# Optimization experiments

Hardware: AMD Instinct MI355X
Metric: run time of the kernel (lower is better)

## Reference

```python
import jax, jax.numpy as jnp
import numpy as np
from jax import lax

B, F, N, C = 1024, 256, 65536, 1000
SOURCE_CLASSES = 751
TEMP = 0.05
MOMENTUM = 0.2


def setup_inputs() -> dict:
    key = jax.random.key(0)
    k1, k2, k3, k4 = jax.random.split(key, 4)
    inputs = jax.random.normal(k1, (B, F), dtype=jnp.float32)
    # indexes in [1, N] so that (indexes - 1) are all valid -> the boolean mask
    # `inds = indexes >= 0` keeps every row (static shapes under jit)
    indexes = jax.random.randint(k2, (B,), 1, N + 1, dtype=jnp.int32)
    features = jax.random.normal(k3, (N, F), dtype=jnp.float32)
    features = features / jnp.linalg.norm(features, axis=1, keepdims=True)  # bank stores unit rows
    labels = jax.random.randint(k4, (N,), 0, C, dtype=jnp.int32)
    return {"inputs": inputs, "indexes": indexes, "features": features, "labels": labels}


def _forward(inputs, idx, features, labels):
    # F.normalize(inputs, dim=1)
    x = inputs / jnp.linalg.norm(inputs, axis=1, keepdims=True)           # [B, F]
    logits = (x @ features.T) / TEMP                                      # [B, N]
    targets = labels[idx]                                                 # [B]
    # sim.index_add_(0, labels, inputs.t()) -> per-class column sums
    sim = jax.ops.segment_sum(logits.T, labels, num_segments=C)           # [C, B]
    nums = jax.ops.segment_sum(jnp.ones((N,), jnp.float32), labels, num_segments=C)  # [C]
    mask = nums > 0
    sim = sim / jnp.where(mask, nums, 1.0)[:, None]                       # per-class mean
    # masked softmax over classes (faithful to original: plain exp, +eps denominator)
    exps = jnp.exp(sim.T) * mask[None, :].astype(jnp.float32)            # [B, C]
    p = exps / (exps.sum(axis=1, keepdims=True) + 1e-6)
    logp = jnp.log(p + 1e-6)
    # F.nll_loss(..., ignore_index=source_classes-1)
    valid = (targets != SOURCE_CLASSES - 1).astype(jnp.float32)
    nll = -jnp.take_along_axis(logp, targets[:, None], axis=1)[:, 0]
    loss = jnp.sum(nll * valid) / jnp.maximum(valid.sum(), 1.0)
    return loss, x


def reference(inputs, indexes, features, labels):
    idx = indexes - 1
    idx = jnp.where(idx == 5554, SOURCE_CLASSES - 1, idx)  # is_source=True special case
    loss, x = _forward(inputs, idx, features, labels)
    # HM.backward's per-sample sequential momentum scatter update + renorm of the bank.
    # Order-dependent on duplicate indices -> inherently sequential -> lax.scan.
    def step(feats, xy):
        xi, yi = xy
        row = MOMENTUM * feats[yi] + (1.0 - MOMENTUM) * xi
        row = row / jnp.linalg.norm(row)
        return feats.at[yi].set(row), None

    new_features, _ = lax.scan(step, features, (x, idx))
    return loss, new_features
```

## Files before the change

kernel.cpp:

```cpp
#include <hip/hip_runtime.h>
#include <math.h>

#define Bn   1024
#define Fdim 256
#define Nn   65536
#define Cn   1000
#define INV_TEMP 20.0f
#define MOM  0.2f

struct WS {
  float x[Bn * Fdim];
  float meanP[Fdim * Cn];
  float mask[Cn];
  float tExp[Bn];
  int   idx[Bn];
  int   targets[Bn];
  int   offsets[Cn];
  int   cursor[Cn];
  int   list[Nn];
  float meanC[Cn * Fdim];
  int   counts[Cn];
  float sumExp[Bn];
};

__global__ __launch_bounds__(64) void k1_norm(const float* __restrict__ inputs,
                                              const int* __restrict__ indexes,
                                              const int* __restrict__ labels,
                                              float* __restrict__ x,
                                              int* __restrict__ idx, int* __restrict__ targets) {
  int b = blockIdx.x, t = threadIdx.x;
  float4 v = *(const float4*)&inputs[b * Fdim + t * 4];
  float s = v.x * v.x + v.y * v.y + v.z * v.z + v.w * v.w;
#pragma unroll
  for (int o = 32; o > 0; o >>= 1) s += __shfl_xor(s, o, 64);
  float inv = 1.0f / sqrtf(s);
  v.x *= inv; v.y *= inv; v.z *= inv; v.w *= inv;
  *(float4*)&x[b * Fdim + t * 4] = v;
  if (t == 0) {
    int i0 = indexes[b] - 1;
    if (i0 == 5554) i0 = 750;
    idx[b] = i0;
    targets[b] = labels[i0];
  }
}

__global__ __launch_bounds__(256) void k2_count(const int* __restrict__ labels,
                                                int* __restrict__ counts) {
  int t = blockIdx.x * blockDim.x + threadIdx.x;
  int4 l = *(const int4*)&labels[t * 4];
  atomicAdd(&counts[l.x], 1);
  atomicAdd(&counts[l.y], 1);
  atomicAdd(&counts[l.z], 1);
  atomicAdd(&counts[l.w], 1);
}

__global__ void k3_scan(const int* __restrict__ counts, int* __restrict__ offsets,
                        int* __restrict__ cursor) {
  __shared__ int s[1024];
  int t = threadIdx.x;
  int v = (t < Cn) ? counts[t] : 0;
  s[t] = v;
  __syncthreads();
  for (int o = 1; o < 1024; o <<= 1) {
    int a = (t >= o) ? s[t - o] : 0;
    __syncthreads();
    s[t] += a;
    __syncthreads();
  }
  if (t < Cn) {
    int off = s[t] - v;
    offsets[t] = off;
    cursor[t] = off;
  }
}

__global__ __launch_bounds__(256) void k4_fill(const int* __restrict__ labels,
                                               int* __restrict__ cursor,
                                               int* __restrict__ list) {
  int t = blockIdx.x * blockDim.x + threadIdx.x;
  int4 l = *(const int4*)&labels[t * 4];
  int n = t * 4;
  list[atomicAdd(&cursor[l.x], 1)] = n;
  list[atomicAdd(&cursor[l.y], 1)] = n + 1;
  list[atomicAdd(&cursor[l.z], 1)] = n + 2;
  list[atomicAdd(&cursor[l.w], 1)] = n + 3;
}

__global__ __launch_bounds__(256) void k5_fused(const float* __restrict__ features,
                                                const int* __restrict__ list,
                                                const int* __restrict__ labels,
                                                float* __restrict__ meanC,
                                                float* __restrict__ out1) {
  int w = blockIdx.x * 4 + (threadIdx.x >> 6);
  int lane = threadIdx.x & 63;
  int e0 = w * 16;
  float4 acc = {0.f, 0.f, 0.f, 0.f};
  int cur = -1;
#pragma unroll
  for (int bh = 0; bh < 2; bh++) {
    int r[8], cc[8];
#pragma unroll
    for (int j = 0; j < 8; j++) r[j] = list[e0 + bh * 8 + j];
#pragma unroll
    for (int j = 0; j < 8; j++) cc[j] = labels[r[j]];
    float4 v[8];
#pragma unroll
    for (int j = 0; j < 8; j++)
      v[j] = *(const float4*)&features[r[j] * Fdim + lane * 4];
#pragma unroll
    for (int j = 0; j < 8; j++) {
      float* o = &out1[r[j] * Fdim + lane * 4];
      o[0] = v[j].x; o[1] = v[j].y; o[2] = v[j].z; o[3] = v[j].w;
      if (cc[j] != cur) {
        if (cur >= 0) {
          float* p = &meanC[cur * Fdim + lane * 4];
          atomicAdd(p + 0, acc.x); atomicAdd(p + 1, acc.y);
          atomicAdd(p + 2, acc.z); atomicAdd(p + 3, acc.w);
        }
        acc.x = 0.f; acc.y = 0.f; acc.z = 0.f; acc.w = 0.f;
        cur = cc[j];
      }
      acc.x += v[j].x; acc.y += v[j].y; acc.z += v[j].z; acc.w += v[j].w;
    }
  }
  float* p = &meanC[cur * Fdim + lane * 4];
  atomicAdd(p + 0, acc.x); atomicAdd(p + 1, acc.y);
  atomicAdd(p + 2, acc.z); atomicAdd(p + 3, acc.w);
}

__global__ __launch_bounds__(256) void k5t_pack(const float* __restrict__ meanC,
                                                const int* __restrict__ counts,
                                                float* __restrict__ meanP,
                                                float* __restrict__ mask) {
  int c = blockIdx.x, t = threadIdx.x;
  int cnt = counts[c];
  float rc = (cnt > 0) ? 1.0f / (float)cnt : 0.f;
  float s = meanC[c * Fdim + t];
  meanP[((t >> 2) * Cn + c) * 4 + (t & 3)] = s * rc;
  if (t == 0) mask[c] = (cnt > 0) ? 1.f : 0.f;
}

#define BBT 4
__global__ __launch_bounds__(256) void k6_matmul(const float* __restrict__ x,
                                                 const float* __restrict__ meanP,
                                                 const float* __restrict__ mask,
                                                 const int* __restrict__ targets,
                                                 float* __restrict__ sumExp,
                                                 float* __restrict__ tExp) {
  int b0 = blockIdx.x * BBT;
  int c  = blockIdx.y * 256 + threadIdx.x;
  int lane = threadIdx.x & 63;
  bool cv = (c < Cn);
  int cc = cv ? c : 0;
  float acc[BBT];
#pragma unroll
  for (int bb = 0; bb < BBT; bb++) acc[bb] = 0.f;
  const float* xb = x + b0 * Fdim;
#pragma unroll 4
  for (int f4 = 0; f4 < Fdim / 4; f4++) {
    float4 mv = *(const float4*)&meanP[(f4 * Cn + cc) * 4];
#pragma unroll
    for (int bb = 0; bb < BBT; bb++) {
      float4 xv = *(const float4*)&xb[bb * Fdim + f4 * 4];
      acc[bb] = fmaf(xv.x, mv.x, acc[bb]);
      acc[bb] = fmaf(xv.y, mv.y, acc[bb]);
      acc[bb] = fmaf(xv.z, mv.z, acc[bb]);
      acc[bb] = fmaf(xv.w, mv.w, acc[bb]);
    }
  }
  float msk = cv ? mask[cc] : 0.f;
#pragma unroll
  for (int bb = 0; bb < BBT; bb++) {
    float e = msk * __expf(acc[bb] * INV_TEMP);
    float s = e;
#pragma unroll
    for (int o = 32; o > 0; o >>= 1) s += __shfl_down(s, o, 64);
    if (lane == 0) atomicAdd(&sumExp[b0 + bb], s);
    int tgt = targets[b0 + bb];
    if (cv && tgt == c) tExp[b0 + bb] = e;
  }
}

__global__ __launch_bounds__(256) void k8_update(const float* __restrict__ features,
                                                 const float* __restrict__ x,
                                                 const int* __restrict__ idx,
                                                 const float* __restrict__ sumExp,
                                                 const float* __restrict__ tExp,
                                                 const int* __restrict__ targets,
                                                 float* __restrict__ out,
                                                 float* __restrict__ out1) {
  int t = threadIdx.x;
  if (blockIdx.x == 256) {
    float a = 0.f, bsum = 0.f;
#pragma unroll
    for (int k = 0; k < 4; k++) {
      int b = t + k * 256;
      float S = sumExp[b], tE = tExp[b];
      float nll = -logf(tE / (S + 1e-6f) + 1e-6f);
      float valid = (targets[b] != 750) ? 1.f : 0.f;
      a += nll * valid; bsum += valid;
    }
#pragma unroll
    for (int o = 32; o > 0; o >>= 1) {
      a += __shfl_down(a, o, 64);
      bsum += __shfl_down(bsum, o, 64);
    }
    __shared__ float ra[4], rb[4];
    if ((t & 63) == 0) { ra[t >> 6] = a; rb[t >> 6] = bsum; }
    __syncthreads();
    if (t == 0) {
      float sa = ra[0] + ra[1] + ra[2] + ra[3];
      float sb = rb[0] + rb[1] + rb[2] + rb[3];
      out[0] = sa / fmaxf(sb, 1.f);
    }
    return;
  }
  __shared__ int ilds[Bn];
  for (int i = t; i < Bn; i += 256) ilds[i] = idx[i];
  __syncthreads();
  int wid = t >> 6, lane = t & 63;
  int b = blockIdx.x * 4 + wid;
  int y = ilds[b];
  for (int base = 0; base < b; base += 64) {
    int j = base + lane;
    bool hit = (j < b) && (ilds[j] == y);
    if (__any(hit)) return;
  }
  float4 r = *(const float4*)&features[y * Fdim + lane * 4];
  for (int base = (b >> 6) << 6; base < Bn; base += 64) {
    int k = base + lane;
    bool hit = (k >= b) && (ilds[k] == y);
    unsigned long long mbits = __ballot(hit);
    while (mbits) {
      int p = __ffsll(mbits) - 1;
      mbits &= mbits - 1;
      int kk = base + p;
      float4 xv = *(const float4*)&x[kk * Fdim + lane * 4];
      r.x = MOM * r.x + (1.f - MOM) * xv.x;
      r.y = MOM * r.y + (1.f - MOM) * xv.y;
      r.z = MOM * r.z + (1.f - MOM) * xv.z;
      r.w = MOM * r.w + (1.f - MOM) * xv.w;
      float ss = r.x * r.x + r.y * r.y + r.z * r.z + r.w * r.w;
#pragma unroll
      for (int o = 32; o > 0; o >>= 1) ss += __shfl_xor(ss, o, 64);
      float inv = 1.0f / sqrtf(ss);
      r.x *= inv; r.y *= inv; r.z *= inv; r.w *= inv;
    }
  }
  int base2 = y * Fdim + lane * 4;
  out1[base2 + 0] = r.x;
  out1[base2 + 1] = r.y;
  out1[base2 + 2] = r.z;
  out1[base2 + 3] = r.w;
}

extern "C" void kernel_launch(void* const* d_in, const int* in_sizes, int n_in,
                              void* d_out, int out_size, void* d_ws, size_t ws_size,
                              hipStream_t stream) {
  const float* inputs   = (const float*)d_in[0];
  const int*   indexes  = (const int*)d_in[1];
  const float* features = (const float*)d_in[2];
  const int*   labels   = (const int*)d_in[3];
  float* out = (float*)d_out;
  WS* w = (WS*)d_ws;

  hipMemsetAsync(w->meanC, 0, (size_t)(Cn * Fdim + Cn + Bn) * 4, stream);
  k1_norm<<<Bn, 64, 0, stream>>>(inputs, indexes, labels, w->x, w->idx, w->targets);
  k2_count<<<Nn / 1024, 256, 0, stream>>>(labels, w->counts);
  k3_scan<<<1, 1024, 0, stream>>>(w->counts, w->offsets, w->cursor);
  k4_fill<<<Nn / 1024, 256, 0, stream>>>(labels, w->cursor, w->list);
  k5_fused<<<Nn / 64, 256, 0, stream>>>(features, w->list, labels, w->meanC, out + 1);
  k5t_pack<<<Cn, 256, 0, stream>>>(w->meanC, w->counts, w->meanP, w->mask);
  k6_matmul<<<dim3(Bn / BBT, 4), 256, 0, stream>>>(w->x, w->meanP, w->mask, w->targets,
                                                   w->sumExp, w->tExp);
  k8_update<<<Bn / 4 + 1, 256, 0, stream>>>(features, w->x, w->idx, w->sumExp, w->tExp,
                                            w->targets, out, out + 1);
}
```

Before: 196.6 us.

## Fuse label counting into normalize, scatter class sums directly into packed layout

Label counting moves into the normalization kernel, which has Bn*64 = Nn threads, so the separate count kernel goes away. The fused gather kernel now atomically accumulates class sums straight into the packed [F/4][C][4] layout used by the matmul. This removes the separate pack kernel and its intermediate buffer. The 1/count scale and the mask are folded into the exp scaling inside the matmul, and the matmul batch tile grows from 4 to 8. In exchange, the atomics now write to strided addresses, and the memset region layout changes.

New measurement: 275.3 us. 40.0% more time.

```diff
diff --git a/kernel.cpp b/kernel.cpp
--- a/kernel.cpp
+++ b/kernel.cpp
@@ -10,15 +10,13 @@
 
 struct WS {
   float x[Bn * Fdim];
-  float meanP[Fdim * Cn];
-  float mask[Cn];
   float tExp[Bn];
   int   idx[Bn];
   int   targets[Bn];
   int   offsets[Cn];
   int   cursor[Cn];
   int   list[Nn];
-  float meanC[Cn * Fdim];
+  float meanP[Fdim * Cn];
   int   counts[Cn];
   float sumExp[Bn];
 };
@@ -27,8 +25,10 @@
                                               const int* __restrict__ indexes,
                                               const int* __restrict__ labels,
                                               float* __restrict__ x,
-                                              int* __restrict__ idx, int* __restrict__ targets) {
+                                              int* __restrict__ idx, int* __restrict__ targets,
+                                              int* __restrict__ counts) {
   int b = blockIdx.x, t = threadIdx.x;
+  atomicAdd(&counts[labels[b * 64 + t]], 1);
   float4 v = *(const float4*)&inputs[b * Fdim + t * 4];
   float s = v.x * v.x + v.y * v.y + v.z * v.z + v.w * v.w;
 #pragma unroll
@@ -42,16 +42,6 @@
     idx[b] = i0;
     targets[b] = labels[i0];
   }
-}
-
-__global__ __launch_bounds__(256) void k2_count(const int* __restrict__ labels,
-                                                int* __restrict__ counts) {
-  int t = blockIdx.x * blockDim.x + threadIdx.x;
-  int4 l = *(const int4*)&labels[t * 4];
-  atomicAdd(&counts[l.x], 1);
-  atomicAdd(&counts[l.y], 1);
-  atomicAdd(&counts[l.z], 1);
-  atomicAdd(&counts[l.w], 1);
 }
 
 __global__ void k3_scan(const int* __restrict__ counts, int* __restrict__ offsets,
@@ -89,61 +79,48 @@
 __global__ __launch_bounds__(256) void k5_fused(const float* __restrict__ features,
                                                 const int* __restrict__ list,
                                                 const int* __restrict__ labels,
-                                                float* __restrict__ meanC,
+                                                float* __restrict__ meanP,
                                                 float* __restrict__ out1) {
   int w = blockIdx.x * 4 + (threadIdx.x >> 6);
   int lane = threadIdx.x & 63;
   int e0 = w * 16;
+  int r[16], cc[16];
+#pragma unroll
+  for (int j = 0; j < 16; j++) r[j] = list[e0 + j];
+#pragma unroll
+  for (int j = 0; j < 16; j++) cc[j] = labels[r[j]];
   float4 acc = {0.f, 0.f, 0.f, 0.f};
-  int cur = -1;
+  int cur = cc[0];
 #pragma unroll
   for (int bh = 0; bh < 2; bh++) {
-    int r[8], cc[8];
-#pragma unroll
-    for (int j = 0; j < 8; j++) r[j] = list[e0 + bh * 8 + j];
-#pragma unroll
-    for (int j = 0; j < 8; j++) cc[j] = labels[r[j]];
     float4 v[8];
 #pragma unroll
     for (int j = 0; j < 8; j++)
-      v[j] = *(const float4*)&features[r[j] * Fdim + lane * 4];
+      v[j] = *(const float4*)&features[(size_t)r[bh * 8 + j] * Fdim + lane * 4];
 #pragma unroll
     for (int j = 0; j < 8; j++) {
-      float* o = &out1[r[j] * Fdim + lane * 4];
+      int e = bh * 8 + j;
+      float* o = &out1[(size_t)r[e] * Fdim + lane * 4];
       o[0] = v[j].x; o[1] = v[j].y; o[2] = v[j].z; o[3] = v[j].w;
-      if (cc[j] != cur) {
-        if (cur >= 0) {
-          float* p = &meanC[cur * Fdim + lane * 4];
-          atomicAdd(p + 0, acc.x); atomicAdd(p + 1, acc.y);
-          atomicAdd(p + 2, acc.z); atomicAdd(p + 3, acc.w);
-        }
+      if (cc[e] != cur) {
+        float* p = &meanP[((size_t)lane * Cn + cur) * 4];
+        atomicAdd(p + 0, acc.x); atomicAdd(p + 1, acc.y);
+        atomicAdd(p + 2, acc.z); atomicAdd(p + 3, acc.w);
         acc.x = 0.f; acc.y = 0.f; acc.z = 0.f; acc.w = 0.f;
-        cur = cc[j];
+        cur = cc[e];
       }
       acc.x += v[j].x; acc.y += v[j].y; acc.z += v[j].z; acc.w += v[j].w;
     }
   }
-  float* p = &meanC[cur * Fdim + lane * 4];
+  float* p = &meanP[((size_t)lane * Cn + cur) * 4];
   atomicAdd(p + 0, acc.x); atomicAdd(p + 1, acc.y);
   atomicAdd(p + 2, acc.z); atomicAdd(p + 3, acc.w);
 }
 
-__global__ __launch_bounds__(256) void k5t_pack(const float* __restrict__ meanC,
-                                                const int* __restrict__ counts,
-                                                float* __restrict__ meanP,
-                                                float* __restrict__ mask) {
-  int c = blockIdx.x, t = threadIdx.x;
-  int cnt = counts[c];
-  float rc = (cnt > 0) ? 1.0f / (float)cnt : 0.f;
-  float s = meanC[c * Fdim + t];
-  meanP[((t >> 2) * Cn + c) * 4 + (t & 3)] = s * rc;
-  if (t == 0) mask[c] = (cnt > 0) ? 1.f : 0.f;
-}
-
-#define BBT 4
+#define BBT 8
 __global__ __launch_bounds__(256) void k6_matmul(const float* __restrict__ x,
                                                  const float* __restrict__ meanP,
-                                                 const float* __restrict__ mask,
+                                                 const int* __restrict__ counts,
                                                  const int* __restrict__ targets,
                                                  float* __restrict__ sumExp,
                                                  float* __restrict__ tExp) {
@@ -168,10 +145,12 @@
       acc[bb] = fmaf(xv.w, mv.w, acc[bb]);
     }
   }
-  float msk = cv ? mask[cc] : 0.f;
+  int cnt = counts[cc];
+  bool live = cv && (cnt > 0);
+  float scale = live ? (INV_TEMP / (float)cnt) : 0.f;
 #pragma unroll
   for (int bb = 0; bb < BBT; bb++) {
-    float e = msk * __expf(acc[bb] * INV_TEMP);
+    float e = live ? __expf(acc[bb] * scale) : 0.f;
     float s = e;
 #pragma unroll
     for (int o = 32; o > 0; o >>= 1) s += __shfl_down(s, o, 64);
@@ -264,14 +243,13 @@
   float* out = (float*)d_out;
   WS* w = (WS*)d_ws;
 
-  hipMemsetAsync(w->meanC, 0, (size_t)(Cn * Fdim + Cn + Bn) * 4, stream);
-  k1_norm<<<Bn, 64, 0, stream>>>(inputs, indexes, labels, w->x, w->idx, w->targets);
-  k2_count<<<Nn / 1024, 256, 0, stream>>>(labels, w->counts);
+  hipMemsetAsync(w->meanP, 0, (size_t)(Fdim * Cn + Cn + Bn) * 4, stream);
+  k1_norm<<<Bn, 64, 0, stream>>>(inputs, indexes, labels, w->x, w->idx, w->targets,
+                                 w->counts);
   k3_scan<<<1, 1024, 0, stream>>>(w->counts, w->offsets, w->cursor);
   k4_fill<<<Nn / 1024, 256, 0, stream>>>(labels, w->cursor, w->list);
-  k5_fused<<<Nn / 64, 256, 0, stream>>>(features, w->list, labels, w->meanC, out + 1);
-  k5t_pack<<<Cn, 256, 0, stream>>>(w->meanC, w->counts, w->meanP, w->mask);
-  k6_matmul<<<dim3(Bn / BBT, 4), 256, 0, stream>>>(w->x, w->meanP, w->mask, w->targets,
+  k5_fused<<<Nn / 64, 256, 0, stream>>>(features, w->list, labels, w->meanP, out + 1);
+  k6_matmul<<<dim3(Bn / BBT, 4), 256, 0, stream>>>(w->x, w->meanP, w->counts, w->targets,
                                                    w->sumExp, w->tExp);
   k8_update<<<Bn / 4 + 1, 256, 0, stream>>>(features, w->x, w->idx, w->sumExp, w->tExp,
                                             w->targets, out, out + 1);
```
